# Optimization experiments

Hardware: AMD Instinct MI355X
Metric: run time of the kernel (lower is better)

## Reference

```python
import jax, jax.numpy as jnp
import numpy as np

D_MODEL = 1024
NUM_HEADS = 16
HEAD_DIM = D_MODEL // NUM_HEADS
ROPE_BASE = 10000.0


def _rotate_half(x):
    x1, x2 = jnp.split(x, 2, axis=-1)
    return jnp.concatenate([-x2, x1], axis=-1)


def _rope_cache(seq_len, head_dim, dtype):
    half = head_dim // 2
    inv_freq = 1.0 / (ROPE_BASE ** (jnp.arange(half, dtype=jnp.float32) / float(half)))
    t = jnp.arange(seq_len, dtype=jnp.float32)
    freqs = t[:, None] * inv_freq[None, :]          # [s, half]
    emb = jnp.concatenate([freqs, freqs], axis=-1)   # [s, head_dim]
    cos = jnp.cos(emb)[None, None, :, :].astype(dtype)  # [1,1,s,d]
    sin = jnp.sin(emb)[None, None, :, :].astype(dtype)
    return cos, sin


def setup_inputs() -> dict:
    key = jax.random.key(0)
    k1, k2, k3 = jax.random.split(key, 3)
    b, s = 4, 2048
    x = jax.random.normal(k1, (b, s, D_MODEL), dtype=jnp.float32)
    mask = jnp.ones((b, s), dtype=jnp.float32)
    Wqkv = jax.random.normal(k2, (D_MODEL, 3 * D_MODEL), dtype=jnp.float32) * (D_MODEL ** -0.5)
    Wout = jax.random.normal(k3, (D_MODEL, D_MODEL), dtype=jnp.float32) * (D_MODEL ** -0.5)
    return {"x": x, "mask": mask, "Wqkv": Wqkv, "Wout": Wout}


def reference(x, mask, Wqkv, Wout):
    b, s, _ = x.shape
    qkv = x @ Wqkv                                   # [b,s,3*d_model]
    q, k, v = jnp.split(qkv, 3, axis=-1)

    def split_heads(t):
        return t.reshape(b, s, NUM_HEADS, HEAD_DIM).transpose(0, 2, 1, 3)  # [b,h,s,d]

    q, k, v = map(split_heads, (q, k, v))
    cos, sin = _rope_cache(s, HEAD_DIM, x.dtype)
    q = q * cos + _rotate_half(q) * sin
    k = k * cos + _rotate_half(k) * sin

    scale = HEAD_DIM ** -0.5
    logits = jnp.einsum('bhid,bhjd->bhij', q, k) * scale
    logits = logits + (1.0 - mask)[:, None, None, :] * -1e9
    attn = jax.nn.softmax(logits, axis=-1)
    out = jnp.einsum('bhij,bhjd->bhid', attn, v)     # [b,h,s,d]
    out = out.transpose(0, 2, 1, 3).reshape(b, s, D_MODEL)
    return out @ Wout
```

## Files before the change

kernel.cpp:

```cpp
#include <hip/hip_runtime.h>

typedef unsigned short u16;
typedef unsigned int u32;
typedef int i32x2 __attribute__((ext_vector_type(2)));
typedef float f32x4 __attribute__((ext_vector_type(4)));
typedef float f32x16 __attribute__((ext_vector_type(16)));
typedef __bf16 bf16x8 __attribute__((ext_vector_type(8)));
typedef unsigned short u16x8 __attribute__((ext_vector_type(8)));
typedef unsigned short u16x4 __attribute__((ext_vector_type(4)));
typedef unsigned int u32x4 __attribute__((ext_vector_type(4)));

#define S_ 2048
#define DM 1024

#define LDS_U32(p) ((__attribute__((address_space(3))) unsigned int*)(p))
#define GLB_U32(p) ((const __attribute__((address_space(1))) unsigned int*)(p))

__device__ __forceinline__ u16 f2bf(float f) {
    unsigned int u = __float_as_uint(f);
    u += 0x7fffu + ((u >> 16) & 1u);
    return (u16)(u >> 16);
}
__device__ __forceinline__ float bf2f(u16 s) {
    return __uint_as_float(((unsigned int)s) << 16);
}
__device__ __forceinline__ float fast_exp2(float x) {
#if __has_builtin(__builtin_amdgcn_exp2f)
    return __builtin_amdgcn_exp2f(x);
#else
    return __expf(x * 0.69314718056f);
#endif
}

__global__ __launch_bounds__(256) void f32_to_bf16_kernel(const float* __restrict__ in,
                                                          u16* __restrict__ o, int n) {
    int i = (blockIdx.x * 256 + threadIdx.x) << 2;
    if (i >= n) return;
    float4 f = *(const float4*)&in[i];
    u16x4 r;
    r[0] = f2bf(f.x); r[1] = f2bf(f.y); r[2] = f2bf(f.z); r[3] = f2bf(f.w);
    *(u16x4*)&o[i] = r;
}

__global__ __launch_bounds__(256) void transpose_w(const float* __restrict__ W,
                                                   u16* __restrict__ Wt, int K, int N) {
    __shared__ float tile[32][33];
    int nb = blockIdx.x << 5, kb = blockIdx.y << 5;
    int tx = threadIdx.x & 31, ty = threadIdx.x >> 5;
#pragma unroll
    for (int r = 0; r < 32; r += 8)
        tile[ty + r][tx] = W[(size_t)(kb + ty + r) * N + nb + tx];
    __syncthreads();
#pragma unroll
    for (int r = 0; r < 32; r += 8)
        Wt[(size_t)(nb + ty + r) * K + kb + tx] = f2bf(tile[tx][ty + r]);
}

template <int MODE>
__global__ __launch_bounds__(256) void gemm_bt(const u16* __restrict__ A,
                                               const u16* __restrict__ Bt,
                                               float* __restrict__ Cf,
                                               u16* __restrict__ Qp, u16* __restrict__ Kp,
                                               u16* __restrict__ Vtp,
                                               int M, int N, int K) {
    __shared__ __align__(16) u16 Al[128 * 32];
    __shared__ __align__(16) u16 Bl[128 * 32];
    const int tid = threadIdx.x;
    const int Ntiles = N >> 7;
    const int cpx = gridDim.x >> 3;
    const int bid = (int)blockIdx.x;
    const int wg = (bid & 7) * cpx + (bid >> 3);
    const int mt = wg / Ntiles, nt = wg % Ntiles;
    const int m0 = mt << 7, n0 = nt << 7;
    const int wave = tid >> 6, lane = tid & 63;
    const int wm = (wave >> 1) << 6, wn = (wave & 1) << 6;
    const int lr = lane & 15, lk = (lane >> 4) << 3;

    const int srow = (wave << 4) + (lane >> 2);
    const int scol = (lane & 3) << 3;

    f32x4 acc[4][4] = {};

    for (int k0 = 0; k0 < K; k0 += 32) {
        __syncthreads();
#pragma unroll
        for (int i = 0; i < 2; ++i) {
            const u16* ga = &A[(size_t)(m0 + srow + (i << 6)) * K + k0 + scol];
            const u16* gb = &Bt[(size_t)(n0 + srow + (i << 6)) * K + k0 + scol];
            __builtin_amdgcn_global_load_lds(GLB_U32(ga), LDS_U32(&Al[(wave << 9) + (i << 11)]), 16, 0, 0);
            __builtin_amdgcn_global_load_lds(GLB_U32(gb), LDS_U32(&Bl[(wave << 9) + (i << 11)]), 16, 0, 0);
        }
        __syncthreads();
        bf16x8 af[4], bfr[4];
#pragma unroll
        for (int i = 0; i < 4; ++i) {
            af[i]  = __builtin_bit_cast(bf16x8, *(const u16x8*)&Al[(wm + (i << 4) + lr) * 32 + lk]);
            bfr[i] = __builtin_bit_cast(bf16x8, *(const u16x8*)&Bl[(wn + (i << 4) + lr) * 32 + lk]);
        }
#pragma unroll
        for (int i = 0; i < 4; ++i)
#pragma unroll
            for (int j = 0; j < 4; ++j)
                acc[i][j] = __builtin_amdgcn_mfma_f32_16x16x32_bf16(af[i], bfr[j], acc[i][j], 0, 0, 0);
    }

    if (MODE == 0) {
        const int t = (n0 + wn) >> 10;
        if (t < 2) {
            const float LN1E4_32 = 9.210340371976184f / 32.0f;
            const float invf0 = __expf(-(float)lr * LN1E4_32);
            const float invf1 = __expf(-(float)(lr + 16) * LN1E4_32);
#pragma unroll
            for (int i = 0; i < 4; ++i) {
                const int rbase = m0 + wm + (i << 4) + ((lane >> 4) << 2);
#pragma unroll
                for (int jj = 0; jj < 4; ++jj) {
                    const float s = (float)((rbase + jj) & (S_ - 1));
                    float sn0, c0, sn1, c1;
                    __sincosf(s * invf0, &sn0, &c0);
                    __sincosf(s * invf1, &sn1, &c1);
                    const float v0 = acc[i][0][jj], v1 = acc[i][1][jj];
                    const float v2 = acc[i][2][jj], v3 = acc[i][3][jj];
                    acc[i][0][jj] = v0 * c0 - v2 * sn0;
                    acc[i][2][jj] = v2 * c0 + v0 * sn0;
                    acc[i][1][jj] = v1 * c1 - v3 * sn1;
                    acc[i][3][jj] = v3 * c1 + v1 * sn1;
                }
            }
            u16* P = (t == 0) ? Qp : Kp;
#pragma unroll
            for (int i = 0; i < 4; ++i) {
#pragma unroll
                for (int j = 0; j < 4; ++j) {
                    int rbase = m0 + wm + (i << 4) + ((lane >> 4) << 2);
                    int col = n0 + wn + (j << 4) + lr;
                    int h = (col & 1023) >> 6, d = col & 63;
#pragma unroll
                    for (int jj = 0; jj < 4; ++jj) {
                        int row = rbase + jj;
                        int b = row >> 11, s = row & 2047;
                        P[((size_t)((b << 4) + h) * S_ + s) * 64 + d] = f2bf(acc[i][j][jj]);
                    }
                }
            }
        } else {
#pragma unroll
            for (int i = 0; i < 4; ++i) {
                const int rbase = m0 + wm + (i << 4) + ((lane >> 4) << 2);
                const int b = rbase >> 11, sb = rbase & 2047;
#pragma unroll
                for (int j = 0; j < 4; ++j) {
                    int col = n0 + wn + (j << 4) + lr;
                    int h = (col & 1023) >> 6, d = col & 63;
                    u16x4 pk;
#pragma unroll
                    for (int jj = 0; jj < 4; ++jj) pk[jj] = f2bf(acc[i][j][jj]);
                    *(u16x4*)&Vtp[((size_t)((b << 4) + h) * 64 + d) * S_ + sb] = pk;
                }
            }
        }
    } else {
#pragma unroll
        for (int i = 0; i < 4; ++i)
#pragma unroll
            for (int j = 0; j < 4; ++j) {
                int rbase = m0 + wm + (i << 4) + ((lane >> 4) << 2);
                int col = n0 + wn + (j << 4) + lr;
#pragma unroll
                for (int jj = 0; jj < 4; ++jj)
                    Cf[(size_t)(rbase + jj) * N + col] = acc[i][j][jj];
            }
    }
}

__device__ __forceinline__ void softmax_chain(f32x16* p, f32x16* acc, f32x16& accS,
                                              float& m_run, u32* wa, u32* wb,
                                              const float* madd_tile, bool hasmask,
                                              float* bcast_w, int c, int hi) {
    if (hasmask) {
#pragma unroll
        for (int tt = 0; tt < 2; ++tt)
#pragma unroll
            for (int rq = 0; rq < 4; ++rq) {
                float4 mf = *(const float4*)&madd_tile[tt * 32 + rq * 8 + hi * 4];
                p[tt][4 * rq + 0] += mf.x;
                p[tt][4 * rq + 1] += mf.y;
                p[tt][4 * rq + 2] += mf.z;
                p[tt][4 * rq + 3] += mf.w;
            }
    }

    float tm[16];
#pragma unroll
    for (int r = 0; r < 16; ++r) tm[r] = fmaxf(p[0][r], p[1][r]);
    float a0 = fmaxf(fmaxf(tm[0], tm[1]), tm[2]);
    float a1 = fmaxf(fmaxf(tm[3], tm[4]), tm[5]);
    float a2 = fmaxf(fmaxf(tm[6], tm[7]), tm[8]);
    float a3 = fmaxf(fmaxf(tm[9], tm[10]), tm[11]);
    float a4 = fmaxf(fmaxf(tm[12], tm[13]), tm[14]);
    float b0 = fmaxf(fmaxf(a0, a1), a2);
    float b1 = fmaxf(fmaxf(a3, a4), tm[15]);
    float mx = fmaxf(b0, b1);
    {
        i32x2 mm = __builtin_amdgcn_permlane32_swap(__float_as_int(mx), __float_as_int(mx), false, false);
        mx = fmaxf(__int_as_float(mm[0]), __int_as_float(mm[1]));
    }

    if (!__all(mx - m_run <= 8.0f)) {
        float mnew = fmaxf(m_run, mx);
        float alpha = fast_exp2(m_run - mnew);
        m_run = mnew;
        bcast_w[c] = alpha;
        float avf[16];
#pragma unroll
        for (int rq = 0; rq < 4; ++rq) {
            float4 t4 = *(const float4*)&bcast_w[rq * 8 + hi * 4];
            avf[4 * rq + 0] = t4.x; avf[4 * rq + 1] = t4.y;
            avf[4 * rq + 2] = t4.z; avf[4 * rq + 3] = t4.w;
        }
#pragma unroll
        for (int r = 0; r < 16; ++r) {
            acc[0][r] *= avf[r];
            acc[1][r] *= avf[r];
            accS[r]   *= avf[r];
        }
    }

#pragma unroll
    for (int tt = 0; tt < 2; ++tt)
#pragma unroll
        for (int r = 0; r < 16; ++r)
            p[tt][r] = fast_exp2(p[tt][r] - m_run);

#pragma unroll
    for (int tt = 0; tt < 2; ++tt)
#pragma unroll
        for (int rq = 0; rq < 4; ++rq) {
            float e0 = p[tt][4 * rq + 0], e1 = p[tt][4 * rq + 1];
            float e2 = p[tt][4 * rq + 2], e3 = p[tt][4 * rq + 3];
            u32 w0, w1;
            asm("v_cvt_pk_bf16_f32 %0, %1, %2" : "=v"(w0) : "v"(e0), "v"(e1));
            asm("v_cvt_pk_bf16_f32 %0, %1, %2" : "=v"(w1) : "v"(e2), "v"(e3));
            wa[4 * tt + rq] = w0;
            wb[4 * tt + rq] = w1;
        }
}

__global__ __launch_bounds__(256, 2) void attn_kernel(const u16* __restrict__ q,
                                                      const u16* __restrict__ k,
                                                      const u16* __restrict__ vt,
                                                      const float* __restrict__ mask,
                                                      u16* __restrict__ outp) {
    __shared__ __align__(16) u16 Kl[2][64 * 64];
    __shared__ __align__(16) u16 Vl[2][64 * 64];
    __shared__ float madd2[2][64];
    __shared__ float bcast[4][32];

    const int tid = threadIdx.x, wave = tid >> 6, lane = tid & 63;
    const int c = lane & 31, hi = lane >> 5, c7 = c & 7;
    const int bh = blockIdx.x & 63, qt = blockIdx.x >> 6;
    const int b = bh >> 4, h = bh & 15;
    const size_t base = (size_t)bh * (S_ * 64);
    const int qrowA = (qt << 8) + (wave << 5) + c;
    const int qrowB = qrowA + 128;

    const float QS = 0.18033688f;

    bf16x8 qfA[4], qfB[4];
#pragma unroll
    for (int j = 0; j < 4; ++j) {
        u16x8 rawA = *(const u16x8*)&q[base + (size_t)qrowA * 64 + j * 16 + hi * 8];
        u16x8 rawB = *(const u16x8*)&q[base + (size_t)qrowB * 64 + j * 16 + hi * 8];
        u16x8 scA, scB;
#pragma unroll
        for (int e = 0; e < 8; ++e) {
            scA[e] = f2bf(bf2f(rawA[e]) * QS);
            scB[e] = f2bf(bf2f(rawB[e]) * QS);
        }
        qfA[j] = __builtin_bit_cast(bf16x8, scA);
        qfB[j] = __builtin_bit_cast(bf16x8, scB);
    }

    u16x8 ou;
#pragma unroll
    for (int e = 0; e < 8; ++e) ou[e] = 0x3F80;
    const bf16x8 onesf = __builtin_bit_cast(bf16x8, ou);

    f32x16 accA[2] = {}, accB[2] = {};
    f32x16 accSA = {}, accSB = {};
    float m_runA = -1e30f, m_runB = -1e30f;

    const int sr = tid >> 2, su = (tid & 3) << 1;
    const int so0 = sr * 64 + ((su ^ (sr & 7)) << 3);
    const int so1 = sr * 64 + (((su + 1) ^ (sr & 7)) << 3);

    u16x8 kc0 = *(const u16x8*)&k[base + (size_t)sr * 64 + su * 8];
    u16x8 kc1 = *(const u16x8*)&k[base + (size_t)sr * 64 + su * 8 + 8];
    u16x8 vc0 = *(const u16x8*)&vt[base + (size_t)sr * S_ + su * 8];
    u16x8 vc1 = *(const u16x8*)&vt[base + (size_t)sr * S_ + su * 8 + 8];
    float mval = (tid < 64) ? mask[b * S_ + tid] : 1.0f;

    for (int t = 0; t < 32; ++t) {
        const int bi = t & 1;
        u16* Kb = &Kl[bi][0];
        u16* Vb = &Vl[bi][0];
        *(u16x8*)&Kb[so0] = kc0;
        *(u16x8*)&Kb[so1] = kc1;
        *(u16x8*)&Vb[so0] = vc0;
        *(u16x8*)&Vb[so1] = vc1;
        if (tid < 64) madd2[bi][tid] = (1.0f - mval) * -1.44269504e9f;
        if (t + 1 < 32) {
            const int kn = (t + 1) << 6;
            kc0 = *(const u16x8*)&k[base + (size_t)(kn + sr) * 64 + su * 8];
            kc1 = *(const u16x8*)&k[base + (size_t)(kn + sr) * 64 + su * 8 + 8];
            vc0 = *(const u16x8*)&vt[base + (size_t)sr * S_ + kn + su * 8];
            vc1 = *(const u16x8*)&vt[base + (size_t)sr * S_ + kn + su * 8 + 8];
            mval = (tid < 64) ? mask[b * S_ + kn + tid] : 1.0f;
        }
        __syncthreads();

        f32x16 pA[2] = {}, pB[2] = {};
        __builtin_amdgcn_s_setprio(1);
#pragma unroll
        for (int j = 0; j < 4; ++j) {
            const int uo = ((2 * j + hi) ^ c7) << 3;
            bf16x8 ka  = __builtin_bit_cast(bf16x8, *(const u16x8*)&Kb[c * 64 + uo]);
            bf16x8 kb2 = __builtin_bit_cast(bf16x8, *(const u16x8*)&Kb[(32 + c) * 64 + uo]);
            pA[0] = __builtin_amdgcn_mfma_f32_32x32x16_bf16(ka,  qfA[j], pA[0], 0, 0, 0);
            pA[1] = __builtin_amdgcn_mfma_f32_32x32x16_bf16(kb2, qfA[j], pA[1], 0, 0, 0);
            pB[0] = __builtin_amdgcn_mfma_f32_32x32x16_bf16(ka,  qfB[j], pB[0], 0, 0, 0);
            pB[1] = __builtin_amdgcn_mfma_f32_32x32x16_bf16(kb2, qfB[j], pB[1], 0, 0, 0);
        }
        __builtin_amdgcn_s_setprio(0);

        bool hasmask = __any(madd2[bi][lane] != 0.0f);

        u32 waA[8], wbA[8], waB[8], wbB[8];
        softmax_chain(pA, accA, accSA, m_runA, waA, wbA, &madd2[bi][0], hasmask, &bcast[wave][0], c, hi);
        softmax_chain(pB, accB, accSB, m_runB, waB, wbB, &madd2[bi][0], hasmask, &bcast[wave][0], c, hi);

        __builtin_amdgcn_s_setprio(1);
#pragma unroll
        for (int ks = 0; ks < 4; ++ks) {
            i32x2 raA = __builtin_amdgcn_permlane32_swap((int)waA[2 * ks], (int)waA[2 * ks + 1], false, false);
            i32x2 rbA = __builtin_amdgcn_permlane32_swap((int)wbA[2 * ks], (int)wbA[2 * ks + 1], false, false);
            i32x2 raB = __builtin_amdgcn_permlane32_swap((int)waB[2 * ks], (int)waB[2 * ks + 1], false, false);
            i32x2 rbB = __builtin_amdgcn_permlane32_swap((int)wbB[2 * ks], (int)wbB[2 * ks + 1], false, false);
            u32x4 pwA, pwB;
            pwA[0] = (u32)raA[0]; pwA[1] = (u32)rbA[0]; pwA[2] = (u32)raA[1]; pwA[3] = (u32)rbA[1];
            pwB[0] = (u32)raB[0]; pwB[1] = (u32)rbB[0]; pwB[2] = (u32)raB[1]; pwB[3] = (u32)rbB[1];
            bf16x8 pafA = __builtin_bit_cast(bf16x8, pwA);
            bf16x8 pafB = __builtin_bit_cast(bf16x8, pwB);
            accSA = __builtin_amdgcn_mfma_f32_32x32x16_bf16(pafA, onesf, accSA, 0, 0, 0);
            accSB = __builtin_amdgcn_mfma_f32_32x32x16_bf16(pafB, onesf, accSB, 0, 0, 0);
            const int uo = ((2 * ks + hi) ^ c7) << 3;
#pragma unroll
            for (int dt = 0; dt < 2; ++dt) {
                bf16x8 vf = __builtin_bit_cast(bf16x8,
                            *(const u16x8*)&Vb[(32 * dt + c) * 64 + uo]);
                accA[dt] = __builtin_amdgcn_mfma_f32_32x32x16_bf16(pafA, vf, accA[dt], 0, 0, 0);
                accB[dt] = __builtin_amdgcn_mfma_f32_32x32x16_bf16(pafB, vf, accB[dt], 0, 0, 0);
            }
        }
        __builtin_amdgcn_s_setprio(0);
    }

    {
        const size_t orow0 = (size_t)b * S_ + (qt << 8) + (wave << 5);
#pragma unroll
        for (int dt = 0; dt < 2; ++dt)
#pragma unroll
            for (int r = 0; r < 16; ++r) {
                int qr = (r & 3) + 8 * (r >> 2) + 4 * hi;
                outp[(orow0 + qr) * DM + h * 64 + dt * 32 + c] =
                    f2bf(accA[dt][r] * __builtin_amdgcn_rcpf(accSA[r]));
            }
    }
    {
        const size_t orow0 = (size_t)b * S_ + (qt << 8) + (wave << 5) + 128;
#pragma unroll
        for (int dt = 0; dt < 2; ++dt)
#pragma unroll
            for (int r = 0; r < 16; ++r) {
                int qr = (r & 3) + 8 * (r >> 2) + 4 * hi;
                outp[(orow0 + qr) * DM + h * 64 + dt * 32 + c] =
                    f2bf(accB[dt][r] * __builtin_amdgcn_rcpf(accSB[r]));
            }
    }
}

extern "C" void kernel_launch(void* const* d_in, const int* in_sizes, int n_in,
                              void* d_out, int out_size, void* d_ws, size_t ws_size,
                              hipStream_t stream) {
    const float* x    = (const float*)d_in[0];
    const float* mask = (const float*)d_in[1];
    const float* Wqkv = (const float*)d_in[2];
    const float* Wout = (const float*)d_in[3];
    float* out = (float*)d_out;
    char* ws = (char*)d_ws;
    const size_t MB = 1u << 20;
    u16* xb    = (u16*)(ws);
    u16* WqkvT = (u16*)(ws + 16 * MB);
    u16* WoutT = (u16*)(ws + 22 * MB);
    u16* qb    = (u16*)(ws + 24 * MB);
    u16* kb    = (u16*)(ws + 40 * MB);
    u16* vtb   = (u16*)(ws + 56 * MB);
    u16* ao    = xb;

    f32_to_bf16_kernel<<<8192, 256, 0, stream>>>(x, xb, 8192 * 1024);
    transpose_w<<<dim3(96, 32), 256, 0, stream>>>(Wqkv, WqkvT, 1024, 3072);
    transpose_w<<<dim3(32, 32), 256, 0, stream>>>(Wout, WoutT, 1024, 1024);
    gemm_bt<0><<<64 * 24, 256, 0, stream>>>(xb, WqkvT, nullptr, qb, kb, vtb, 8192, 3072, 1024);
    attn_kernel<<<512, 256, 0, stream>>>(qb, kb, vtb, mask, ao);
    gemm_bt<1><<<64 * 8, 256, 0, stream>>>(ao, WoutT, out, nullptr, nullptr, nullptr, 8192, 1024, 1024);
}
```

Baseline: 218.5 us.

## Replace 128x128 GEMM with pipelined 256x256 tile kernel using swizzled LDS

```diff
diff --git a/kernel.cpp b/kernel.cpp
--- a/kernel.cpp
+++ b/kernel.cpp
@@ -56,52 +56,94 @@
         Wt[(size_t)(nb + ty + r) * K + kb + tx] = f2bf(tile[tx][ty + r]);
 }
 
+
+#define ABLK(B, KK) ((B) * 32768 + (KK) * 8192)
+#define BBLK(B, KK) ((B) * 32768 + 16384 + (KK) * 8192)
+
 template <int MODE>
-__global__ __launch_bounds__(256) void gemm_bt(const u16* __restrict__ A,
-                                               const u16* __restrict__ Bt,
-                                               float* __restrict__ Cf,
-                                               u16* __restrict__ Qp, u16* __restrict__ Kp,
-                                               u16* __restrict__ Vtp,
-                                               int M, int N, int K) {
-    __shared__ __align__(16) u16 Al[128 * 32];
-    __shared__ __align__(16) u16 Bl[128 * 32];
-    const int tid = threadIdx.x;
-    const int Ntiles = N >> 7;
+__global__ __launch_bounds__(512, 2) void gemm256(const u16* __restrict__ A,
+                                                  const u16* __restrict__ Bt,
+                                                  float* __restrict__ Cf,
+                                                  u16* __restrict__ Qp, u16* __restrict__ Kp,
+                                                  u16* __restrict__ Vtp,
+                                                  int M, int N, int K) {
+    __shared__ __align__(16) u16 lds[65536];
+    const int tid = threadIdx.x, wave = tid >> 6, lane = tid & 63;
+    const int Ntiles = N >> 8;
     const int cpx = gridDim.x >> 3;
     const int bid = (int)blockIdx.x;
     const int wg = (bid & 7) * cpx + (bid >> 3);
     const int mt = wg / Ntiles, nt = wg % Ntiles;
-    const int m0 = mt << 7, n0 = nt << 7;
-    const int wave = tid >> 6, lane = tid & 63;
-    const int wm = (wave >> 1) << 6, wn = (wave & 1) << 6;
-    const int lr = lane & 15, lk = (lane >> 4) << 3;
-
-    const int srow = (wave << 4) + (lane >> 2);
-    const int scol = (lane & 3) << 3;
-
-    f32x4 acc[4][4] = {};
-
-    for (int k0 = 0; k0 < K; k0 += 32) {
-        __syncthreads();
-#pragma unroll
-        for (int i = 0; i < 2; ++i) {
-            const u16* ga = &A[(size_t)(m0 + srow + (i << 6)) * K + k0 + scol];
-            const u16* gb = &Bt[(size_t)(n0 + srow + (i << 6)) * K + k0 + scol];
-            __builtin_amdgcn_global_load_lds(GLB_U32(ga), LDS_U32(&Al[(wave << 9) + (i << 11)]), 16, 0, 0);
-            __builtin_amdgcn_global_load_lds(GLB_U32(gb), LDS_U32(&Bl[(wave << 9) + (i << 11)]), 16, 0, 0);
-        }
-        __syncthreads();
-        bf16x8 af[4], bfr[4];
-#pragma unroll
-        for (int i = 0; i < 4; ++i) {
-            af[i]  = __builtin_bit_cast(bf16x8, *(const u16x8*)&Al[(wm + (i << 4) + lr) * 32 + lk]);
-            bfr[i] = __builtin_bit_cast(bf16x8, *(const u16x8*)&Bl[(wn + (i << 4) + lr) * 32 + lk]);
-        }
-#pragma unroll
-        for (int i = 0; i < 4; ++i)
-#pragma unroll
-            for (int j = 0; j < 4; ++j)
-                acc[i][j] = __builtin_amdgcn_mfma_f32_16x16x32_bf16(af[i], bfr[j], acc[i][j], 0, 0, 0);
+    const int m0 = mt << 8, n0 = nt << 8;
+    const int wm = (wave >> 2) << 7, wn = (wave & 3) << 6;
+    const int lr = lane & 15, lu = lane >> 4;
+
+    const int NT = K >> 6;
+    const int NIT = K >> 7;
+
+    f32x4 acc[8][4] = {};
+
+    const int srow0 = wave * 16 + (lane >> 2);
+    const int scole = (((lane & 3) ^ ((lane >> 3) & 3)) << 3);
+
+#define STAGE(BLK, MAT, ROW0, KCOL)                                                           \
+    {                                                                                         \
+        _Pragma("unroll") for (int l = 0; l < 2; ++l) {                                       \
+            const u16* src = &(MAT)[(size_t)((ROW0) + srow0 + l * 128) * K + (KCOL) + scole];  \
+            __builtin_amdgcn_global_load_lds(GLB_U32(src),                                    \
+                LDS_U32(&lds[(BLK) + l * 4096 + wave * 512]), 16, 0, 0);                      \
+        }                                                                                     \
+    }
+
+#define LDFRAG(BLK, ROW) \
+    __builtin_bit_cast(bf16x8, *(const u16x8*)&lds[(BLK) + (ROW) * 32 + ((lu ^ (((ROW) >> 1) & 3)) << 3)])
+
+#define PHASE(BUF, IH, KK, LOADB, SBLK, SMAT, SROW0, SKT, SKK, DOVM_END)                  \
+    {                                                                                     \
+        _Pragma("unroll") for (int ii = 0; ii < 4; ++ii) {                                \
+            int row = wm + ((IH) * 4 + ii) * 16 + lr;                                     \
+            af[ii] = LDFRAG(ABLK(BUF, KK), row);                                          \
+        }                                                                                 \
+        if (LOADB) {                                                                      \
+            _Pragma("unroll") for (int j = 0; j < 4; ++j) {                               \
+                int row = wn + j * 16 + lr;                                               \
+                bfv[j] = LDFRAG(BBLK(BUF, KK), row);                                      \
+            }                                                                             \
+        }                                                                                 \
+        STAGE(SBLK, SMAT, SROW0, (((SKT) & (NT - 1)) << 6) + ((SKK) << 5));               \
+        asm volatile("s_barrier" ::: "memory");                                           \
+        asm volatile("s_waitcnt lgkmcnt(0)" ::: "memory");                                \
+        __builtin_amdgcn_sched_barrier(0);                                                \
+        __builtin_amdgcn_s_setprio(1);                                                    \
+        _Pragma("unroll") for (int ii = 0; ii < 4; ++ii)                                  \
+            _Pragma("unroll") for (int j = 0; j < 4; ++j)                                 \
+                acc[(IH) * 4 + ii][j] = __builtin_amdgcn_mfma_f32_16x16x32_bf16(          \
+                    af[ii], bfv[j], acc[(IH) * 4 + ii][j], 0, 0, 0);                      \
+        __builtin_amdgcn_s_setprio(0);                                                    \
+        if (DOVM_END) asm volatile("s_waitcnt vmcnt(8)" ::: "memory");                    \
+        asm volatile("s_barrier" ::: "memory");                                           \
+    }
+
+    STAGE(ABLK(0, 0), A, m0, 0);
+    STAGE(BBLK(0, 0), Bt, n0, 0);
+    STAGE(ABLK(0, 1), A, m0, 32);
+    STAGE(BBLK(0, 1), Bt, n0, 32);
+    STAGE(ABLK(1, 0), A, m0, 64);
+    STAGE(BBLK(1, 0), Bt, n0, 64);
+    asm volatile("s_waitcnt vmcnt(8)" ::: "memory");
+    asm volatile("s_barrier" ::: "memory");
+
+    for (int t = 0; t < NIT; ++t) {
+        const int kt = 2 * t;
+        bf16x8 af[4], bfv[4];
+        PHASE(0, 0, 0, true,  ABLK(1, 1), A,  m0, kt + 1, 1, false);
+        PHASE(0, 1, 0, false, BBLK(1, 1), Bt, n0, kt + 1, 1, true);
+        PHASE(0, 0, 1, true,  ABLK(0, 0), A,  m0, kt + 2, 0, false);
+        PHASE(0, 1, 1, false, BBLK(0, 0), Bt, n0, kt + 2, 0, true);
+        PHASE(1, 0, 0, true,  ABLK(0, 1), A,  m0, kt + 2, 1, false);
+        PHASE(1, 1, 0, false, BBLK(0, 1), Bt, n0, kt + 2, 1, true);
+        PHASE(1, 0, 1, true,  ABLK(1, 0), A,  m0, kt + 3, 0, false);
+        PHASE(1, 1, 1, false, BBLK(1, 0), Bt, n0, kt + 3, 0, true);
     }
 
     if (MODE == 0) {
@@ -111,7 +153,7 @@
             const float invf0 = __expf(-(float)lr * LN1E4_32);
             const float invf1 = __expf(-(float)(lr + 16) * LN1E4_32);
 #pragma unroll
-            for (int i = 0; i < 4; ++i) {
+            for (int i = 0; i < 8; ++i) {
                 const int rbase = m0 + wm + (i << 4) + ((lane >> 4) << 2);
 #pragma unroll
                 for (int jj = 0; jj < 4; ++jj) {
@@ -129,7 +171,7 @@
             }
             u16* P = (t == 0) ? Qp : Kp;
 #pragma unroll
-            for (int i = 0; i < 4; ++i) {
+            for (int i = 0; i < 8; ++i) {
 #pragma unroll
                 for (int j = 0; j < 4; ++j) {
                     int rbase = m0 + wm + (i << 4) + ((lane >> 4) << 2);
@@ -145,7 +187,7 @@
             }
         } else {
 #pragma unroll
-            for (int i = 0; i < 4; ++i) {
+            for (int i = 0; i < 8; ++i) {
                 const int rbase = m0 + wm + (i << 4) + ((lane >> 4) << 2);
                 const int b = rbase >> 11, sb = rbase & 2047;
 #pragma unroll
@@ -161,7 +203,7 @@
         }
     } else {
 #pragma unroll
-        for (int i = 0; i < 4; ++i)
+        for (int i = 0; i < 8; ++i)
 #pragma unroll
             for (int j = 0; j < 4; ++j) {
                 int rbase = m0 + wm + (i << 4) + ((lane >> 4) << 2);
@@ -171,6 +213,9 @@
                     Cf[(size_t)(rbase + jj) * N + col] = acc[i][j][jj];
             }
     }
+#undef PHASE
+#undef LDFRAG
+#undef STAGE
 }
 
 __device__ __forceinline__ void softmax_chain(f32x16* p, f32x16* acc, f32x16& accS,
@@ -410,7 +455,7 @@
     f32_to_bf16_kernel<<<8192, 256, 0, stream>>>(x, xb, 8192 * 1024);
     transpose_w<<<dim3(96, 32), 256, 0, stream>>>(Wqkv, WqkvT, 1024, 3072);
     transpose_w<<<dim3(32, 32), 256, 0, stream>>>(Wout, WoutT, 1024, 1024);
-    gemm_bt<0><<<64 * 24, 256, 0, stream>>>(xb, WqkvT, nullptr, qb, kb, vtb, 8192, 3072, 1024);
+    gemm256<0><<<32 * 12, 512, 0, stream>>>(xb, WqkvT, nullptr, qb, kb, vtb, 8192, 3072, 1024);
     attn_kernel<<<512, 256, 0, stream>>>(qb, kb, vtb, mask, ao);
-    gemm_bt<1><<<64 * 8, 256, 0, stream>>>(ao, WoutT, out, nullptr, nullptr, nullptr, 8192, 1024, 1024);
-}
+    gemm256<1><<<32 * 4, 512, 0, stream>>>(ao, WoutT, out, nullptr, nullptr, nullptr, 8192, 1024, 1024);
+}
```

Result: faster. 210.7 us (-3.5%).
